# Performance work log

Hardware: AMD Instinct MI355X
Metric: run time of the kernel (lower is better)

The kernel has to match this reference:

```python
import jax, jax.numpy as jnp
import numpy as np

A = 16          # n_agents
H = 128         # rnn_hidden_dim
IN = 128        # input_shape
NA = 32         # n_attention
NACT = 14       # n_actions
TAU = 0.5       # gumbel_softmax_tau
B_ENV = 1024    # parallel envs
BZ = B_ENV * A

# neighbor index: for agent i, all j != i (matches select_ind in torch code)
IDX = np.array([[j for j in range(A) if j != i] for i in range(A)])  # [A, A-1]


def gru_cell(x, h, Wih, Whh, bih, bhh):
    # torch GRUCell gate order: r, z, n
    gi = x @ Wih.T + bih
    gh = h @ Whh.T + bhh
    ir, iz, inn = jnp.split(gi, 3, axis=-1)
    hr, hz, hn = jnp.split(gh, 3, axis=-1)
    r = jax.nn.sigmoid(ir + hr)
    z = jax.nn.sigmoid(iz + hz)
    n = jnp.tanh(inn + r * hn)
    return (1.0 - z) * n + z * h


def run_gru(seq, Wih, Whh, bih, bhh):
    # seq: [T, N, D]; returns all hidden states [T, N, H]
    h0 = jnp.zeros((seq.shape[1], Whh.shape[1]), seq.dtype)
    def step(h, x):
        h2 = gru_cell(x, h, Wih, Whh, bih, bhh)
        return h2, h2
    _, ys = jax.lax.scan(step, h0, seq)
    return ys


def setup_inputs() -> dict:
    key = jax.random.key(0)
    ks = jax.random.split(key, 24)
    def u(k, shape, fan):
        s = 1.0 / np.sqrt(fan)
        return jax.random.uniform(k, shape, jnp.float32, -s, s)
    inp = {
        "inputs": jax.random.normal(ks[0], (BZ, IN), jnp.float32),
        "hidden_state": jax.random.normal(ks[1], (BZ, H), jnp.float32),
        "gumbel_u": jax.random.uniform(ks[2], (BZ * (A - 1), 2), jnp.float32),
        # fc1
        "W1": u(ks[3], (H, IN), IN), "b1": u(ks[4], (H,), IN),
        # GRUCell
        "Wih_c": u(ks[5], (3 * H, H), H), "Whh_c": u(ks[6], (3 * H, H), H),
        "bih_c": u(ks[7], (3 * H,), H), "bhh_c": u(ks[8], (3 * H,), H),
        # bi-GRU forward dir (input 2H)
        "Wih_f": u(ks[9], (3 * H, 2 * H), H), "Whh_f": u(ks[10], (3 * H, H), H),
        "bih_f": u(ks[11], (3 * H,), H), "bhh_f": u(ks[12], (3 * H,), H),
        # bi-GRU backward dir
        "Wih_b": u(ks[13], (3 * H, 2 * H), H), "Whh_b": u(ks[14], (3 * H, H), H),
        "bih_b": u(ks[15], (3 * H,), H), "bhh_b": u(ks[16], (3 * H,), H),
        # hard classifier
        "Wc": u(ks[17], (2, 2 * H), 2 * H), "bc": u(ks[18], (2,), 2 * H),
        # attention projections (no bias)
        "Wq": u(ks[19], (NA, H), H), "Wk": u(ks[20], (NA, H), H),
        # fc2
        "W2": u(ks[21], (NACT, 2 * H), 2 * H), "b2": u(ks[22], (NACT,), 2 * H),
    }
    return inp


def reference(inputs, hidden_state, gumbel_u, W1, b1, Wih_c, Whh_c, bih_c, bhh_c,
              Wih_f, Whh_f, bih_f, bhh_f, Wih_b, Whh_b, bih_b, bhh_b,
              Wc, bc, Wq, Wk, W2, b2):
    bz = inputs.shape[0]
    B = bz // A
    x1 = jax.nn.relu(inputs @ W1.T + b1)
    h_rnn = gru_cell(x1, hidden_state.reshape(-1, H), Wih_c, Whh_c, bih_c, bhh_c)  # [bz, H]

    h3 = h_rnn.reshape(B, A, H)
    nbr = h3[:, IDX, :]                                           # [B, A, A-1, H]
    self_rep = jnp.broadcast_to(h3[:, :, None, :], (B, A, A - 1, H))
    pairs = jnp.concatenate([self_rep, nbr], axis=-1)             # [B, A, A-1, 2H]
    seq = pairs.transpose(2, 0, 1, 3).reshape(A - 1, bz, 2 * H)   # [T, bz, 2H]

    yf = run_gru(seq, Wih_f, Whh_f, bih_f, bhh_f)
    yb = jnp.flip(run_gru(jnp.flip(seq, 0), Wih_b, Whh_b, bih_b, bhh_b), 0)
    h_hard = jnp.concatenate([yf, yb], axis=-1)                   # [T, bz, 2H]
    h_hard = h_hard.transpose(1, 0, 2).reshape(-1, 2 * H)         # [bz*T, 2H]

    logits = h_hard @ Wc.T + bc                                   # [bz*T, 2]
    g = -jnp.log(-jnp.log(gumbel_u + 1e-10) + 1e-10)
    gs = jax.nn.softmax((logits + g) / TAU, axis=-1)
    hard_w = gs[:, 1].reshape(B, A, A - 1)                        # hard gate

    q = (h_rnn @ Wq.T).reshape(B, A, NA)
    k = (h_rnn @ Wk.T).reshape(B, A, NA)
    kn = k[:, IDX, :] * hard_w[..., None]                         # [B, A, A-1, NA]
    scores = jnp.einsum('bad,bamd->bam', q, kn) / np.sqrt(NA)
    soft_w = jax.nn.softmax(scores, axis=-1)                      # [B, A, A-1]

    w = hard_w * soft_w
    agg = jnp.einsum('bam,bamh->bah', w, nbr).reshape(bz, H)
    out = jnp.concatenate([h_rnn, agg], axis=-1) @ W2.T + b2      # [bz, n_actions]
    return out, h_rnn
```

## Files before the change

kernel.cpp:

```cpp
#include <hip/hip_runtime.h>
#include <hip/hip_bf16.h>


typedef __attribute__((ext_vector_type(8))) short short8;
typedef __attribute__((ext_vector_type(4))) short short4v;
typedef __attribute__((ext_vector_type(4))) float float4v;
typedef __attribute__((ext_vector_type(2))) unsigned long long ull2;

#define BF2F(x) __bfloat162float(x)
typedef __hip_bfloat16 bf;

__device__ __forceinline__ float frcp(float x) {
  return __builtin_amdgcn_rcpf(x);
}
__device__ __forceinline__ float fsigmoid(float x) {
  return frcp(1.f + __expf(-x));
}
__device__ __forceinline__ float ftanh(float x) {
  float e = __expf(2.f * x);
  return 1.f - 2.f * frcp(1.f + e);
}
__device__ __forceinline__ float rdv(const void* p, int i, int f) {
  return f ? ((const float*)p)[i] : BF2F(((const bf*)p)[i]);
}
__device__ __forceinline__ float upk(unsigned long long v, int s) {
  union { unsigned int i; float f; } x;
  x.i = ((unsigned int)((v >> s) & 0xffffULL)) << 16;
  return x.f;
}

static const int AO[23] = {
  0, 2097152, 4194304, 4685824, 4702208, 4702336, 4751488, 4800640, 4801024,
  4801408, 4899712, 4948864, 4949248, 4949632, 5047936, 5097088, 5097472,
  5097856, 5098368, 5098384, 5102480, 5106576, 5110160};
static const int AN[23] = {
  2097152, 2097152, 491520, 16384, 128, 49152, 49152, 384, 384, 98304, 49152,
  384, 384, 98304, 49152, 384, 384, 512, 2, 4096, 4096, 3584, 14};

struct CArgs {
  const void* src[23];
  int n[23];
  int off[23];
};

__global__ void kDetect(const unsigned short* __restrict__ p, int* flag) {
  __shared__ int s;
  if (threadIdx.x == 0) s = 0;
  __syncthreads();
  int hit = 0;
  for (int i = threadIdx.x; i < 4096; i += 1024) {
    int e = (p[i] >> 7) & 0xFF;
    if (e >= 0xC0) hit = 1;
  }
  if (hit) atomicOr(&s, 1);
  __syncthreads();
  if (threadIdx.x == 0) *flag = s;
}

__global__ void kConvert(CArgs a, const int* __restrict__ flag,
                         bf* __restrict__ arena,
                         const void* __restrict__ WqR, const void* __restrict__ WkR,
                         const void* __restrict__ W2R, const void* __restrict__ WcR,
                         bf* __restrict__ Wqk, bf* __restrict__ W2p,
                         bf* __restrict__ Wcb) {
  const int b = blockIdx.y;
  const int f = *flag;
  if (b == 23) {
    int idx = blockIdx.x * 256 + threadIdx.x;
    if (idx < 8192) {
      int r = idx >> 7, c = idx & 127;
      float v = (r < 32) ? rdv(WqR, r * 128 + c, f) : rdv(WkR, (r - 32) * 128 + c, f);
      Wqk[idx] = __float2bfloat16(v);
    }
    if (idx < 4096)
      W2p[idx] = __float2bfloat16((idx < 3584) ? rdv(W2R, idx, f) : 0.f);
    if (idx < 512) {
      int dir = idx >> 8, l = (idx >> 7) & 1, k = idx & 127;
      Wcb[idx] = __float2bfloat16(rdv(WcR, l * 256 + dir * 128 + k, f));
    }
    return;
  }
  if (b == 2 || b == 18 || b == 22) return;
  const int n = a.n[b];
  const int nv = n & ~7;
  bf* dst = arena + a.off[b];
  const int gid = blockIdx.x * 256 + threadIdx.x;
  const int gs = gridDim.x * 256;
  if (f) {
    const float* s = (const float*)a.src[b];
    for (int i = gid * 8; i < nv; i += gs * 8) {
      float4 x0 = *(const float4*)(s + i);
      float4 x1 = *(const float4*)(s + i + 4);
      short8 v;
      bf t;
      t = __float2bfloat16(x0.x); v[0] = *(short*)&t;
      t = __float2bfloat16(x0.y); v[1] = *(short*)&t;
      t = __float2bfloat16(x0.z); v[2] = *(short*)&t;
      t = __float2bfloat16(x0.w); v[3] = *(short*)&t;
      t = __float2bfloat16(x1.x); v[4] = *(short*)&t;
      t = __float2bfloat16(x1.y); v[5] = *(short*)&t;
      t = __float2bfloat16(x1.z); v[6] = *(short*)&t;
      t = __float2bfloat16(x1.w); v[7] = *(short*)&t;
      *(short8*)(dst + i) = v;
    }
    for (int i = nv + gid; i < n; i += gs) dst[i] = __float2bfloat16(s[i]);
  } else {
    const short8* s = (const short8*)a.src[b];
    short8* d = (short8*)dst;
    for (int i = gid; i * 8 < nv; i += gs) d[i] = s[i];
    const unsigned short* ss = (const unsigned short*)a.src[b];
    unsigned short* ds = (unsigned short*)dst;
    for (int i = nv + gid; i < n; i += gs) ds[i] = ss[i];
  }
}

__global__ __launch_bounds__(256) void kGemm(const bf* __restrict__ A,
                                             const bf* __restrict__ W,
                                             const bf* __restrict__ bias,
                                             bf* __restrict__ out,
                                             int N, int relu) {
  const int tid = threadIdx.x;
  const int wave = tid >> 6, lane = tid & 63;
  const int quad = lane >> 4, ci = lane & 15;
  const int mr = blockIdx.x * 64 + wave * 16;
  const int nbase = blockIdx.y * 64;
  const int ntiles = (N - nbase < 64) ? ((N - nbase) >> 4) : 4;

  float4v acc[4];
#pragma unroll
  for (int i = 0; i < 4; ++i) acc[i] = {0.f, 0.f, 0.f, 0.f};

#pragma unroll
  for (int ks = 0; ks < 4; ++ks) {
    short8 a = *(const short8*)(A + (size_t)(mr + ci) * 128 + ks * 32 + quad * 8);
    for (int nt = 0; nt < ntiles; ++nt) {
      short8 b = *(const short8*)(W + (size_t)(nbase + nt * 16 + ci) * 128 + ks * 32 + quad * 8);
      acc[nt] = __builtin_amdgcn_mfma_f32_16x16x32_bf16(a, b, acc[nt], 0, 0, 0);
    }
  }

  for (int nt = 0; nt < ntiles; ++nt) {
    int col = nbase + nt * 16 + ci;
    float bv = bias ? BF2F(bias[col]) : 0.f;
#pragma unroll
    for (int r = 0; r < 4; ++r) {
      int row = mr + quad * 4 + r;
      float v = acc[nt][r] + bv;
      if (relu) v = fmaxf(v, 0.f);
      out[(size_t)row * N + col] = __float2bfloat16(v);
    }
  }
}

__global__ __launch_bounds__(256, 4) void kStep(
    const bf* __restrict__ Hp, const bf* __restrict__ Whh,
    const bf* __restrict__ G, int gld,
    const bf* __restrict__ bhh,
    bf* __restrict__ Ho, float* __restrict__ HcopyF) {
  const int half = blockIdx.z;
  const int tid = threadIdx.x;
  const int wave = tid >> 6, lane = tid & 63;
  const int quad = lane >> 4, ci = lane & 15;
  const int mr = blockIdx.x * 64 + wave * 16;

  float4v acc[12];
#pragma unroll
  for (int i = 0; i < 12; ++i) acc[i] = {0.f, 0.f, 0.f, 0.f};

#pragma unroll
  for (int ks = 0; ks < 4; ++ks) {
    short8 a = *(const short8*)(Hp + (size_t)(mr + ci) * 128 + ks * 32 + quad * 8);
#pragma unroll
    for (int g = 0; g < 3; ++g)
#pragma unroll
      for (int nt = 0; nt < 4; ++nt) {
        short8 b = *(const short8*)(Whh + (size_t)(g * 128 + half * 64 + nt * 16 + ci) * 128 + ks * 32 + quad * 8);
        acc[g * 4 + nt] = __builtin_amdgcn_mfma_f32_16x16x32_bf16(a, b, acc[g * 4 + nt], 0, 0, 0);
      }
  }

  float bR[4], bZ[4], bN[4];
#pragma unroll
  for (int nt = 0; nt < 4; ++nt) {
    int c = half * 64 + nt * 16 + ci;
    bR[nt] = BF2F(bhh[c]);
    bZ[nt] = BF2F(bhh[128 + c]);
    bN[nt] = BF2F(bhh[256 + c]);
  }

#pragma unroll
  for (int r = 0; r < 4; ++r) {
    int rr = mr + quad * 4 + r;
    const bf* gs = G + (size_t)rr * gld;
#pragma unroll
    for (int nt = 0; nt < 4; ++nt) {
      int c = half * 64 + nt * 16 + ci;
      float gr = BF2F(gs[c]), gz = BF2F(gs[128 + c]), gnn = BF2F(gs[256 + c]);
      float pre_r = acc[nt][r] + gr + bR[nt];
      float pre_z = acc[4 + nt][r] + gz + bZ[nt];
      float hn_   = acc[8 + nt][r] + bN[nt];
      float rg = fsigmoid(pre_r);
      float zg = fsigmoid(pre_z);
      float ng = ftanh(gnn + rg * hn_);
      float hp = BF2F(Hp[(size_t)rr * 128 + c]);
      float hv = ng + zg * (hp - ng);
      Ho[(size_t)rr * 128 + c] = __float2bfloat16(hv);
      if (HcopyF) HcopyF[(size_t)rr * 128 + c] = hv;
    }
  }
}

__global__ __launch_bounds__(512, 4) void kSeq(
    const bf* __restrict__ hrnn,
    const bf* __restrict__ Wih_f, const bf* __restrict__ Wih_b,
    const bf* __restrict__ Whh_f, const bf* __restrict__ Whh_b,
    const bf* __restrict__ bih_f, const bf* __restrict__ bih_b,
    const bf* __restrict__ bhh_f, const bf* __restrict__ bhh_b,
    const bf* __restrict__ Wcb, float* __restrict__ L) {
  __shared__ unsigned long long sGiN[16][130];
  __shared__ bf sH[2][16][136];
  __shared__ float sL[16][15][2];
  __shared__ bf sWc[2][136];

  const int env = blockIdx.x;
  const int dir = blockIdx.y;
  const int tid = threadIdx.x;
  const int wave = tid >> 6, lane = tid & 63;
  const int nh = wave;
  const int quad = lane >> 4, ci = lane & 15;
  const bf* Wih = dir ? Wih_b : Wih_f;
  const bf* Whh = dir ? Whh_b : Whh_f;
  const bf* bih = dir ? bih_b : bih_f;
  const bf* bhh = dir ? bhh_b : bhh_f;
  const int h0q = nh * 16 + quad * 4;

  float4v gS[3], gN[3];
#pragma unroll
  for (int i = 0; i < 3; ++i) { gS[i] = {0.f, 0.f, 0.f, 0.f}; gN[i] = {0.f, 0.f, 0.f, 0.f}; }
#pragma unroll
  for (int ks = 0; ks < 4; ++ks) {
    short8 bh = *(const short8*)(hrnn + (size_t)(env * 16 + ci) * 128 + ks * 32 + quad * 8);
#pragma unroll
    for (int g = 0; g < 3; ++g) {
      const bf* wrow = Wih + (size_t)(g * 128 + nh * 16 + ci) * 256 + ks * 32 + quad * 8;
      short8 ws = *(const short8*)(wrow);
      short8 wn = *(const short8*)(wrow + 128);
      gS[g] = __builtin_amdgcn_mfma_f32_16x16x32_bf16(ws, bh, gS[g], 0, 0, 0);
      gN[g] = __builtin_amdgcn_mfma_f32_16x16x32_bf16(wn, bh, gN[g], 0, 0, 0);
    }
  }
#pragma unroll
  for (int g = 0; g < 3; ++g)
#pragma unroll
    for (int r = 0; r < 4; ++r) {
      int c = g * 128 + h0q + r;
      float bv = BF2F(bih[c]);
      if (g < 2) bv += BF2F(bhh[c]);
      gS[g][r] += bv;
    }
#pragma unroll
  for (int r = 0; r < 4; ++r) {
    unsigned long long pk = 0;
#pragma unroll
    for (int g = 0; g < 3; ++g) {
      bf b = __float2bfloat16(gN[g][r]);
      pk |= ((unsigned long long)(*(unsigned short*)&b)) << (16 * g);
    }
    sGiN[ci][h0q + r] = pk;
  }

  {
    bf z = __float2bfloat16(0.f);
    bf* p = &sH[0][0][0];
    for (int i = tid; i < 16 * 136; i += 512) p[i] = z;
    if (tid < 256)
      sWc[tid >> 7][tid & 127] = Wcb[(dir * 2 + (tid >> 7)) * 128 + (tid & 127)];
  }

  short8 Bf[12];
#pragma unroll
  for (int g = 0; g < 3; ++g)
#pragma unroll
    for (int ks = 0; ks < 4; ++ks)
      Bf[g * 4 + ks] =
          *(const short8*)(Whh + (size_t)(g * 128 + nh * 16 + ci) * 128 + ks * 32 + quad * 8);

  float bNc[4];
#pragma unroll
  for (int r = 0; r < 4; ++r) bNc[r] = BF2F(bhh[256 + h0q + r]);

  float hPrev[4];
#pragma unroll
  for (int r = 0; r < 4; ++r) hPrev[r] = 0.f;

  __syncthreads();

  for (int t = 0; t < 15; ++t) {
    const int cur = t & 1, nxt = cur ^ 1;
    const int m = dir ? (14 - t) : t;
    const int jr = m + ((m >= ci) ? 1 : 0);

    ull2 nb01 = *(const ull2*)&sGiN[jr][h0q];
    ull2 nb23 = *(const ull2*)&sGiN[jr][h0q + 2];

    float4v acc[3];
#pragma unroll
    for (int i = 0; i < 3; ++i) acc[i] = {0.f, 0.f, 0.f, 0.f};
    float4v lacc = {0.f, 0.f, 0.f, 0.f};
#pragma unroll
    for (int ks = 0; ks < 4; ++ks) {
      short8 bh = *(const short8*)&sH[cur][ci][ks * 32 + quad * 8];
#pragma unroll
      for (int g = 0; g < 3; ++g)
        acc[g] = __builtin_amdgcn_mfma_f32_16x16x32_bf16(Bf[g * 4 + ks], bh, acc[g], 0, 0, 0);
      if (nh == 0) {
        short8 wv = *(const short8*)&sWc[ci & 1][ks * 32 + quad * 8];
        lacc = __builtin_amdgcn_mfma_f32_16x16x32_bf16(wv, bh, lacc, 0, 0, 0);
      }
    }
    if (nh == 0 && t > 0 && quad == 0) {
      int mp = dir ? (15 - t) : (t - 1);
      sL[ci][mp][0] = lacc[0];
      sL[ci][mp][1] = lacc[1];
    }

    short4v hv4;
#pragma unroll
    for (int r = 0; r < 4; ++r) {
      unsigned long long nb = (r == 0) ? nb01.x : (r == 1) ? nb01.y
                             : (r == 2) ? nb23.x : nb23.y;
      float pre_r = acc[0][r] + gS[0][r] + upk(nb, 0);
      float pre_z = acc[1][r] + gS[1][r] + upk(nb, 16);
      float gnn   = gS[2][r] + upk(nb, 32);
      float hn_   = acc[2][r] + bNc[r];
      float rg = fsigmoid(pre_r);
      float zg = fsigmoid(pre_z);
      float ng = ftanh(gnn + rg * hn_);
      float hv = ng + zg * (hPrev[r] - ng);
      hPrev[r] = hv;
      bf b = __float2bfloat16(hv);
      hv4[r] = *(short*)&b;
    }
    *(short4v*)&sH[nxt][ci][h0q] = hv4;
    __syncthreads();
  }

  if (nh == 0) {
    float4v lacc = {0.f, 0.f, 0.f, 0.f};
#pragma unroll
    for (int ks = 0; ks < 4; ++ks) {
      short8 bh = *(const short8*)&sH[1][ci][ks * 32 + quad * 8];
      short8 wv = *(const short8*)&sWc[ci & 1][ks * 32 + quad * 8];
      lacc = __builtin_amdgcn_mfma_f32_16x16x32_bf16(wv, bh, lacc, 0, 0, 0);
    }
    if (quad == 0) {
      int mf = dir ? 0 : 14;
      sL[ci][mf][0] = lacc[0];
      sL[ci][mf][1] = lacc[1];
    }
  }
  __syncthreads();

  for (int i = tid; i < 480; i += 512) {
    int row = i / 30, rem = i - row * 30;
    int mm = rem >> 1, l = rem & 1;
    L[(size_t)((env * 16 + row) * 15 + mm) * 4 + dir * 2 + l] = sL[row][mm][l];
  }
}

__global__ __launch_bounds__(256) void kAttn(
    const bf* __restrict__ h, const bf* __restrict__ Wqk,
    const float* __restrict__ L, const void* __restrict__ guRaw,
    const void* __restrict__ bcRaw, const int* __restrict__ flag,
    bf* __restrict__ aggB) {
  __shared__ float sh[16 * 132];
  __shared__ float sqk[16 * 64];
  __shared__ float shw[16 * 15];
  __shared__ float sw[16 * 16];
  int bb = blockIdx.x, tid = threadIdx.x;
  const int f = *flag;

  {
    const int w = tid >> 6, lane = tid & 63;
    const int quad = lane >> 4, ci = lane & 15;
    float4v acc = {0.f, 0.f, 0.f, 0.f};
#pragma unroll
    for (int ks = 0; ks < 4; ++ks) {
      short8 a_ = *(const short8*)(h + (size_t)(bb * 16 + ci) * 128 + ks * 32 + quad * 8);
      short8 b_ = *(const short8*)(Wqk + (size_t)(w * 16 + ci) * 128 + ks * 32 + quad * 8);
      acc = __builtin_amdgcn_mfma_f32_16x16x32_bf16(a_, b_, acc, 0, 0, 0);
    }
#pragma unroll
    for (int r = 0; r < 4; ++r)
      sqk[(quad * 4 + r) * 64 + w * 16 + ci] = acc[r];
  }
  for (int i = tid; i < 2048; i += 256)
    sh[(i >> 7) * 132 + (i & 127)] = BF2F(h[(size_t)bb * 2048 + i]);
  if (tid < 240) {
    int idx = bb * 240 + tid;
    const float* Lp = L + (size_t)idx * 4;
    float l0 = Lp[0] + Lp[2] + rdv(bcRaw, 0, f);
    float l1 = Lp[1] + Lp[3] + rdv(bcRaw, 1, f);
    float u0 = rdv(guRaw, idx * 2, f);
    float u1 = rdv(guRaw, idx * 2 + 1, f);
    float g0 = -__logf(-__logf(u0 + 1e-10f) + 1e-10f);
    float g1 = -__logf(-__logf(u1 + 1e-10f) + 1e-10f);
    shw[tid] = fsigmoid(((l1 + g1) - (l0 + g0)) * 2.0f);
  }
  __syncthreads();

  int a = tid >> 4, i = tid & 15;
  float s = -1e30f;
  if (i < 15) {
    int j = i + (i >= a);
    float d = 0.f;
#pragma unroll
    for (int c = 0; c < 32; ++c) d += sqk[a * 64 + c] * sqk[j * 64 + 32 + c];
    s = shw[a * 15 + i] * d * 0.17677669529663687f;
  }
  float mx = s;
#pragma unroll
  for (int d = 1; d < 16; d <<= 1) mx = fmaxf(mx, __shfl_xor(mx, d));
  float e = (i < 15) ? __expf(s - mx) : 0.f;
  float sum = e;
#pragma unroll
  for (int d = 1; d < 16; d <<= 1) sum += __shfl_xor(sum, d);
  float w = (i < 15) ? (e * frcp(sum)) * shw[a * 15 + i] : 0.f;
  sw[a * 16 + i] = w;
  __syncthreads();

  float ac[8] = {0, 0, 0, 0, 0, 0, 0, 0};
  for (int mm = 0; mm < 15; ++mm) {
    int jm = mm + (mm >= a);
    float wm = sw[a * 16 + mm];
    const float* shp = &sh[jm * 132 + i * 8];
    float4 h0 = *(const float4*)shp;
    float4 h1 = *(const float4*)(shp + 4);
    ac[0] += wm * h0.x; ac[1] += wm * h0.y; ac[2] += wm * h0.z; ac[3] += wm * h0.w;
    ac[4] += wm * h1.x; ac[5] += wm * h1.y; ac[6] += wm * h1.z; ac[7] += wm * h1.w;
  }
  short8 v;
#pragma unroll
  for (int d = 0; d < 8; ++d) {
    bf b = __float2bfloat16(ac[d]);
    v[d] = *(short*)&b;
  }
  *(short8*)(aggB + (size_t)(bb * 16 + a) * 128 + i * 8) = v;
}

__global__ __launch_bounds__(256) void kGemmOut(
    const bf* __restrict__ hrnn, const bf* __restrict__ aggB,
    const bf* __restrict__ W2p, const void* __restrict__ b2Raw,
    const int* __restrict__ flag, float* __restrict__ out) {
  const int tid = threadIdx.x;
  const int wave = tid >> 6, lane = tid & 63;
  const int quad = lane >> 4, ci = lane & 15;
  const int mr = blockIdx.x * 64 + wave * 16;
  const int f = *flag;

  float4v acc = {0.f, 0.f, 0.f, 0.f};
#pragma unroll
  for (int ks = 0; ks < 8; ++ks) {
    const bf* src = (ks < 4) ? hrnn : aggB;
    int k = (ks & 3) * 32 + quad * 8;
    short8 a = *(const short8*)(src + (size_t)(mr + ci) * 128 + k);
    short8 b = *(const short8*)(W2p + (size_t)ci * 256 + ks * 32 + quad * 8);
    acc = __builtin_amdgcn_mfma_f32_16x16x32_bf16(a, b, acc, 0, 0, 0);
  }

  if (ci < 14) {
    float bv = rdv(b2Raw, ci, f);
#pragma unroll
    for (int r = 0; r < 4; ++r)
      out[(size_t)(mr + quad * 4 + r) * 14 + ci] = acc[r] + bv;
  }
}

extern "C" void kernel_launch(void* const* d_in, const int* in_sizes, int n_in,
                              void* d_out, int out_size, void* d_ws, size_t ws_size,
                              hipStream_t stream) {
  const size_t OFF_ARENA = 0;
  const size_t OFF_FLAG  = 10220544;
  const size_t OFF_A     = 10220800;
  const size_t OFF_WQK   = 26998016;
  const size_t OFF_WCB   = 27014400;
  const size_t OFF_W2P   = 27410944;
  const size_t OFF_HRNN  = 27419136;
  const size_t NEEDED    = 84042240;
  if (ws_size < NEEDED) return;
  if (n_in < 23 || in_sizes[0] != 2097152 || in_sizes[3] != 16384 ||
      in_sizes[5] != 49152 || in_sizes[9] != 98304 || in_sizes[17] != 512 ||
      in_sizes[19] != 4096 || in_sizes[21] != 3584 || out_size != 2326528)
    return;

  char* ws = (char*)d_ws;
  bf*    arena = (bf*)(ws + OFF_ARENA);
  float* L     = (float*)(ws + OFF_ARENA);
  int*   flag  = (int*)(ws + OFF_FLAG);
  bf*    x1    = (bf*)(ws + OFF_A);
  bf*    gi_c  = (bf*)(ws + OFF_A + 4194304);
  bf*    aggB  = (bf*)(ws + OFF_A + 983040);
  bf*    Wqk   = (bf*)(ws + OFF_WQK);
  bf*    Wcb   = (bf*)(ws + OFF_WCB);
  bf*    W2p   = (bf*)(ws + OFF_W2P);
  bf*    hrnn  = (bf*)(ws + OFF_HRNN);

  float* out14 = (float*)d_out;
  float* outh  = (float*)d_out + 229376;

  kDetect<<<1, 1024, 0, stream>>>((const unsigned short*)d_in[0], flag);
  CArgs ca;
  for (int i = 0; i < 23; ++i) { ca.src[i] = d_in[i]; ca.n[i] = AN[i]; ca.off[i] = AO[i]; }
  kConvert<<<dim3(128, 24), 256, 0, stream>>>(ca, flag, arena,
                                              d_in[19], d_in[20], d_in[21], d_in[17],
                                              Wqk, W2p, Wcb);

  const bf* inputs = arena + AO[0];
  const bf* hidden = arena + AO[1];
  const bf* W1     = arena + AO[3];
  const bf* b1     = arena + AO[4];
  const bf* Wih_c  = arena + AO[5];
  const bf* Whh_c  = arena + AO[6];
  const bf* bih_c  = arena + AO[7];
  const bf* bhh_c  = arena + AO[8];
  const bf* Wih_f  = arena + AO[9];
  const bf* Whh_f  = arena + AO[10];
  const bf* bih_f  = arena + AO[11];
  const bf* bhh_f  = arena + AO[12];
  const bf* Wih_b  = arena + AO[13];
  const bf* Whh_b  = arena + AO[14];
  const bf* bih_b  = arena + AO[15];
  const bf* bhh_b  = arena + AO[16];

  kGemm<<<dim3(256, 2), 256, 0, stream>>>(inputs, W1, b1, x1, 128, 1);
  kGemm<<<dim3(256, 6), 256, 0, stream>>>(x1, Wih_c, bih_c, gi_c, 384, 0);
  kStep<<<dim3(256, 1, 2), 256, 0, stream>>>(hidden, Whh_c, gi_c, 384, bhh_c,
                                             hrnn, outh);

  kSeq<<<dim3(1024, 2), 512, 0, stream>>>(hrnn, Wih_f, Wih_b, Whh_f, Whh_b,
                                          bih_f, bih_b, bhh_f, bhh_b, Wcb, L);

  kAttn<<<dim3(1024), 256, 0, stream>>>(hrnn, Wqk, L, d_in[2], d_in[18], flag,
                                        aggB);
  kGemmOut<<<dim3(256), 256, 0, stream>>>(hrnn, aggB, W2p, d_in[22], flag, out14);
}
```

Measured before the change: 280.5 us.

## Fuse detect into convert, fc1 with GRU input GEMM, and attention with output GEMM

Folds the dtype-detection kernel into the convert kernel, where every block recomputes the flag locally. Fuses the fc1 GEMM with ReLU and the GRU input-projection GEMM into one kernel, keeping x1 in LDS. Fuses attention with the final output GEMM, keeping aggregated vectors in LDS and processing four envs per block. This removes three launches and intermediate global round trips, but the attention stage drops from 1024 to 256 blocks and is serialised inside each block.

```diff
diff --git a/kernel.cpp b/kernel.cpp
--- a/kernel.cpp
+++ b/kernel.cpp
@@ -43,28 +43,29 @@
   int off[23];
 };
 
-__global__ void kDetect(const unsigned short* __restrict__ p, int* flag) {
-  __shared__ int s;
-  if (threadIdx.x == 0) s = 0;
-  __syncthreads();
-  int hit = 0;
-  for (int i = threadIdx.x; i < 4096; i += 1024) {
-    int e = (p[i] >> 7) & 0xFF;
-    if (e >= 0xC0) hit = 1;
-  }
-  if (hit) atomicOr(&s, 1);
-  __syncthreads();
-  if (threadIdx.x == 0) *flag = s;
-}
-
-__global__ void kConvert(CArgs a, const int* __restrict__ flag,
+__global__ void kConvert(CArgs a, int* __restrict__ flagOut,
                          bf* __restrict__ arena,
                          const void* __restrict__ WqR, const void* __restrict__ WkR,
                          const void* __restrict__ W2R, const void* __restrict__ WcR,
                          bf* __restrict__ Wqk, bf* __restrict__ W2p,
                          bf* __restrict__ Wcb) {
+  __shared__ int sflag;
+  if (threadIdx.x == 0) sflag = 0;
+  __syncthreads();
+  {
+    const unsigned short* p0 = (const unsigned short*)a.src[0];
+    int hit = 0;
+    for (int i = threadIdx.x; i < 4096; i += 256) {
+      int e = (p0[i] >> 7) & 0xFF;
+      if (e >= 0xC0) hit = 1;
+    }
+    if (hit) atomicOr(&sflag, 1);
+  }
+  __syncthreads();
+  const int f = sflag;
   const int b = blockIdx.y;
-  const int f = *flag;
+  if (b == 0 && blockIdx.x == 0 && threadIdx.x == 0) *flagOut = f;
+
   if (b == 23) {
     int idx = blockIdx.x * 256 + threadIdx.x;
     if (idx < 8192) {
@@ -114,40 +115,63 @@
   }
 }
 
-__global__ __launch_bounds__(256) void kGemm(const bf* __restrict__ A,
-                                             const bf* __restrict__ W,
-                                             const bf* __restrict__ bias,
-                                             bf* __restrict__ out,
-                                             int N, int relu) {
+__global__ __launch_bounds__(256) void kFused12(
+    const bf* __restrict__ inputs, const bf* __restrict__ W1,
+    const bf* __restrict__ b1, const bf* __restrict__ Wih,
+    const bf* __restrict__ bih, bf* __restrict__ gi) {
+  __shared__ bf sX[4][16][136];
   const int tid = threadIdx.x;
   const int wave = tid >> 6, lane = tid & 63;
   const int quad = lane >> 4, ci = lane & 15;
-  const int mr = blockIdx.x * 64 + wave * 16;
-  const int nbase = blockIdx.y * 64;
-  const int ntiles = (N - nbase < 64) ? ((N - nbase) >> 4) : 4;
-
-  float4v acc[4];
-#pragma unroll
-  for (int i = 0; i < 4; ++i) acc[i] = {0.f, 0.f, 0.f, 0.f};
-
+  const int row0 = blockIdx.x * 64 + wave * 16;
+
+  float4v xa[8];
+#pragma unroll
+  for (int i = 0; i < 8; ++i) xa[i] = {0.f, 0.f, 0.f, 0.f};
 #pragma unroll
   for (int ks = 0; ks < 4; ++ks) {
-    short8 a = *(const short8*)(A + (size_t)(mr + ci) * 128 + ks * 32 + quad * 8);
-    for (int nt = 0; nt < ntiles; ++nt) {
-      short8 b = *(const short8*)(W + (size_t)(nbase + nt * 16 + ci) * 128 + ks * 32 + quad * 8);
-      acc[nt] = __builtin_amdgcn_mfma_f32_16x16x32_bf16(a, b, acc[nt], 0, 0, 0);
-    }
-  }
-
-  for (int nt = 0; nt < ntiles; ++nt) {
-    int col = nbase + nt * 16 + ci;
-    float bv = bias ? BF2F(bias[col]) : 0.f;
+    short8 inr = *(const short8*)(inputs + (size_t)(row0 + ci) * 128 + ks * 32 + quad * 8);
+#pragma unroll
+    for (int ct = 0; ct < 8; ++ct) {
+      short8 wfr = *(const short8*)(W1 + (size_t)(ct * 16 + ci) * 128 + ks * 32 + quad * 8);
+      xa[ct] = __builtin_amdgcn_mfma_f32_16x16x32_bf16(wfr, inr, xa[ct], 0, 0, 0);
+    }
+  }
+#pragma unroll
+  for (int ct = 0; ct < 8; ++ct) {
+    short4v v4;
 #pragma unroll
     for (int r = 0; r < 4; ++r) {
-      int row = mr + quad * 4 + r;
-      float v = acc[nt][r] + bv;
-      if (relu) v = fmaxf(v, 0.f);
-      out[(size_t)row * N + col] = __float2bfloat16(v);
+      float v = xa[ct][r] + BF2F(b1[ct * 16 + quad * 4 + r]);
+      v = fmaxf(v, 0.f);
+      bf t = __float2bfloat16(v);
+      v4[r] = *(short*)&t;
+    }
+    *(short4v*)&sX[wave][ci][ct * 16 + quad * 4] = v4;
+  }
+  short8 af[4];
+#pragma unroll
+  for (int ks = 0; ks < 4; ++ks)
+    af[ks] = *(const short8*)&sX[wave][ci][ks * 32 + quad * 8];
+
+  for (int cg = 0; cg < 6; ++cg) {
+    float4v acc[4];
+#pragma unroll
+    for (int i = 0; i < 4; ++i) acc[i] = {0.f, 0.f, 0.f, 0.f};
+#pragma unroll
+    for (int ks = 0; ks < 4; ++ks)
+#pragma unroll
+      for (int nt = 0; nt < 4; ++nt) {
+        short8 b = *(const short8*)(Wih + (size_t)(cg * 64 + nt * 16 + ci) * 128 + ks * 32 + quad * 8);
+        acc[nt] = __builtin_amdgcn_mfma_f32_16x16x32_bf16(af[ks], b, acc[nt], 0, 0, 0);
+      }
+#pragma unroll
+    for (int nt = 0; nt < 4; ++nt) {
+      int col = cg * 64 + nt * 16 + ci;
+      float bv = BF2F(bih[col]);
+#pragma unroll
+      for (int r = 0; r < 4; ++r)
+        gi[(size_t)(row0 + quad * 4 + r) * 384 + col] = __float2bfloat16(acc[nt][r] + bv);
     }
   }
 }
@@ -368,111 +392,116 @@
   }
 }
 
-__global__ __launch_bounds__(256) void kAttn(
+__global__ __launch_bounds__(256) void kTail(
     const bf* __restrict__ h, const bf* __restrict__ Wqk,
     const float* __restrict__ L, const void* __restrict__ guRaw,
     const void* __restrict__ bcRaw, const int* __restrict__ flag,
-    bf* __restrict__ aggB) {
+    const bf* __restrict__ W2p, const void* __restrict__ b2Raw,
+    float* __restrict__ out) {
   __shared__ float sh[16 * 132];
   __shared__ float sqk[16 * 64];
-  __shared__ float shw[16 * 15];
+  __shared__ float shw[240];
   __shared__ float sw[16 * 16];
-  int bb = blockIdx.x, tid = threadIdx.x;
+  __shared__ bf sAgg[64][136];
+  const int b4 = blockIdx.x;
+  const int tid = threadIdx.x;
   const int f = *flag;
+  const int a = tid >> 4, i = tid & 15;
+
+  for (int e = 0; e < 4; ++e) {
+    const int bb = b4 * 4 + e;
+    __syncthreads();
+    {
+      const int w = tid >> 6, lane = tid & 63;
+      const int quad = lane >> 4, ci = lane & 15;
+      float4v acc = {0.f, 0.f, 0.f, 0.f};
+#pragma unroll
+      for (int ks = 0; ks < 4; ++ks) {
+        short8 a_ = *(const short8*)(h + (size_t)(bb * 16 + ci) * 128 + ks * 32 + quad * 8);
+        short8 b_ = *(const short8*)(Wqk + (size_t)(w * 16 + ci) * 128 + ks * 32 + quad * 8);
+        acc = __builtin_amdgcn_mfma_f32_16x16x32_bf16(a_, b_, acc, 0, 0, 0);
+      }
+#pragma unroll
+      for (int r = 0; r < 4; ++r)
+        sqk[(quad * 4 + r) * 64 + w * 16 + ci] = acc[r];
+    }
+    for (int k = tid; k < 2048; k += 256)
+      sh[(k >> 7) * 132 + (k & 127)] = BF2F(h[(size_t)bb * 2048 + k]);
+    if (tid < 240) {
+      int idx = bb * 240 + tid;
+      const float* Lp = L + (size_t)idx * 4;
+      float l0 = Lp[0] + Lp[2] + rdv(bcRaw, 0, f);
+      float l1 = Lp[1] + Lp[3] + rdv(bcRaw, 1, f);
+      float u0 = rdv(guRaw, idx * 2, f);
+      float u1 = rdv(guRaw, idx * 2 + 1, f);
+      float g0 = -__logf(-__logf(u0 + 1e-10f) + 1e-10f);
+      float g1 = -__logf(-__logf(u1 + 1e-10f) + 1e-10f);
+      shw[tid] = fsigmoid(((l1 + g1) - (l0 + g0)) * 2.0f);
+    }
+    __syncthreads();
+
+    float s = -1e30f;
+    if (i < 15) {
+      int j = i + (i >= a);
+      float d = 0.f;
+#pragma unroll
+      for (int c = 0; c < 32; ++c) d += sqk[a * 64 + c] * sqk[j * 64 + 32 + c];
+      s = shw[a * 15 + i] * d * 0.17677669529663687f;
+    }
+    float mx = s;
+#pragma unroll
+    for (int d = 1; d < 16; d <<= 1) mx = fmaxf(mx, __shfl_xor(mx, d));
+    float ex = (i < 15) ? __expf(s - mx) : 0.f;
+    float sum = ex;
+#pragma unroll
+    for (int d = 1; d < 16; d <<= 1) sum += __shfl_xor(sum, d);
+    float w = (i < 15) ? (ex * frcp(sum)) * shw[a * 15 + i] : 0.f;
+    sw[a * 16 + i] = w;
+    __syncthreads();
+
+    float ac[8] = {0, 0, 0, 0, 0, 0, 0, 0};
+    for (int mm = 0; mm < 15; ++mm) {
+      int jm = mm + (mm >= a);
+      float wm = sw[a * 16 + mm];
+      const float* shp = &sh[jm * 132 + i * 8];
+      float4 h0 = *(const float4*)shp;
+      float4 h1 = *(const float4*)(shp + 4);
+      ac[0] += wm * h0.x; ac[1] += wm * h0.y; ac[2] += wm * h0.z; ac[3] += wm * h0.w;
+      ac[4] += wm * h1.x; ac[5] += wm * h1.y; ac[6] += wm * h1.z; ac[7] += wm * h1.w;
+    }
+    short8 v;
+#pragma unroll
+    for (int d = 0; d < 8; ++d) {
+      bf b = __float2bfloat16(ac[d]);
+      v[d] = *(short*)&b;
+    }
+    *(short8*)&sAgg[e * 16 + a][i * 8] = v;
+  }
+  __syncthreads();
 
   {
-    const int w = tid >> 6, lane = tid & 63;
+    const int wave = tid >> 6, lane = tid & 63;
     const int quad = lane >> 4, ci = lane & 15;
+    const int mr = b4 * 64 + wave * 16;
     float4v acc = {0.f, 0.f, 0.f, 0.f};
 #pragma unroll
     for (int ks = 0; ks < 4; ++ks) {
-      short8 a_ = *(const short8*)(h + (size_t)(bb * 16 + ci) * 128 + ks * 32 + quad * 8);
-      short8 b_ = *(const short8*)(Wqk + (size_t)(w * 16 + ci) * 128 + ks * 32 + quad * 8);
+      short8 a_ = *(const short8*)(h + (size_t)(mr + ci) * 128 + ks * 32 + quad * 8);
+      short8 b_ = *(const short8*)(W2p + (size_t)ci * 256 + ks * 32 + quad * 8);
       acc = __builtin_amdgcn_mfma_f32_16x16x32_bf16(a_, b_, acc, 0, 0, 0);
     }
 #pragma unroll
-    for (int r = 0; r < 4; ++r)
-      sqk[(quad * 4 + r) * 64 + w * 16 + ci] = acc[r];
-  }
-  for (int i = tid; i < 2048; i += 256)
-    sh[(i >> 7) * 132 + (i & 127)] = BF2F(h[(size_t)bb * 2048 + i]);
-  if (tid < 240) {
-    int idx = bb * 240 + tid;
-    const float* Lp = L + (size_t)idx * 4;
-    float l0 = Lp[0] + Lp[2] + rdv(bcRaw, 0, f);
-    float l1 = Lp[1] + Lp[3] + rdv(bcRaw, 1, f);
-    float u0 = rdv(guRaw, idx * 2, f);
-    float u1 = rdv(guRaw, idx * 2 + 1, f);
-    float g0 = -__logf(-__logf(u0 + 1e-10f) + 1e-10f);
-    float g1 = -__logf(-__logf(u1 + 1e-10f) + 1e-10f);
-    shw[tid] = fsigmoid(((l1 + g1) - (l0 + g0)) * 2.0f);
-  }
-  __syncthreads();
-
-  int a = tid >> 4, i = tid & 15;
-  float s = -1e30f;
-  if (i < 15) {
-    int j = i + (i >= a);
-    float d = 0.f;
-#pragma unroll
-    for (int c = 0; c < 32; ++c) d += sqk[a * 64 + c] * sqk[j * 64 + 32 + c];
-    s = shw[a * 15 + i] * d * 0.17677669529663687f;
-  }
-  float mx = s;
-#pragma unroll
-  for (int d = 1; d < 16; d <<= 1) mx = fmaxf(mx, __shfl_xor(mx, d));
-  float e = (i < 15) ? __expf(s - mx) : 0.f;
-  float sum = e;
-#pragma unroll
-  for (int d = 1; d < 16; d <<= 1) sum += __shfl_xor(sum, d);
-  float w = (i < 15) ? (e * frcp(sum)) * shw[a * 15 + i] : 0.f;
-  sw[a * 16 + i] = w;
-  __syncthreads();
-
-  float ac[8] = {0, 0, 0, 0, 0, 0, 0, 0};
-  for (int mm = 0; mm < 15; ++mm) {
-    int jm = mm + (mm >= a);
-    float wm = sw[a * 16 + mm];
-    const float* shp = &sh[jm * 132 + i * 8];
-    float4 h0 = *(const float4*)shp;
-    float4 h1 = *(const float4*)(shp + 4);
-    ac[0] += wm * h0.x; ac[1] += wm * h0.y; ac[2] += wm * h0.z; ac[3] += wm * h0.w;
-    ac[4] += wm * h1.x; ac[5] += wm * h1.y; ac[6] += wm * h1.z; ac[7] += wm * h1.w;
-  }
-  short8 v;
-#pragma unroll
-  for (int d = 0; d < 8; ++d) {
-    bf b = __float2bfloat16(ac[d]);
-    v[d] = *(short*)&b;
-  }
-  *(short8*)(aggB + (size_t)(bb * 16 + a) * 128 + i * 8) = v;
-}
-
-__global__ __launch_bounds__(256) void kGemmOut(
-    const bf* __restrict__ hrnn, const bf* __restrict__ aggB,
-    const bf* __restrict__ W2p, const void* __restrict__ b2Raw,
-    const int* __restrict__ flag, float* __restrict__ out) {
-  const int tid = threadIdx.x;
-  const int wave = tid >> 6, lane = tid & 63;
-  const int quad = lane >> 4, ci = lane & 15;
-  const int mr = blockIdx.x * 64 + wave * 16;
-  const int f = *flag;
-
-  float4v acc = {0.f, 0.f, 0.f, 0.f};
-#pragma unroll
-  for (int ks = 0; ks < 8; ++ks) {
-    const bf* src = (ks < 4) ? hrnn : aggB;
-    int k = (ks & 3) * 32 + quad * 8;
-    short8 a = *(const short8*)(src + (size_t)(mr + ci) * 128 + k);
-    short8 b = *(const short8*)(W2p + (size_t)ci * 256 + ks * 32 + quad * 8);
-    acc = __builtin_amdgcn_mfma_f32_16x16x32_bf16(a, b, acc, 0, 0, 0);
-  }
-
-  if (ci < 14) {
-    float bv = rdv(b2Raw, ci, f);
-#pragma unroll
-    for (int r = 0; r < 4; ++r)
-      out[(size_t)(mr + quad * 4 + r) * 14 + ci] = acc[r] + bv;
+    for (int ks = 0; ks < 4; ++ks) {
+      short8 a_ = *(const short8*)&sAgg[wave * 16 + ci][ks * 32 + quad * 8];
+      short8 b_ = *(const short8*)(W2p + (size_t)ci * 256 + 128 + ks * 32 + quad * 8);
+      acc = __builtin_amdgcn_mfma_f32_16x16x32_bf16(a_, b_, acc, 0, 0, 0);
+    }
+    if (ci < 14) {
+      float bv = rdv(b2Raw, ci, f);
+#pragma unroll
+      for (int r = 0; r < 4; ++r)
+        out[(size_t)(mr + quad * 4 + r) * 14 + ci] = acc[r] + bv;
+    }
   }
 }
 
@@ -497,9 +526,7 @@
   bf*    arena = (bf*)(ws + OFF_ARENA);
   float* L     = (float*)(ws + OFF_ARENA);
   int*   flag  = (int*)(ws + OFF_FLAG);
-  bf*    x1    = (bf*)(ws + OFF_A);
   bf*    gi_c  = (bf*)(ws + OFF_A + 4194304);
-  bf*    aggB  = (bf*)(ws + OFF_A + 983040);
   bf*    Wqk   = (bf*)(ws + OFF_WQK);
   bf*    Wcb   = (bf*)(ws + OFF_WCB);
   bf*    W2p   = (bf*)(ws + OFF_W2P);
@@ -508,7 +535,6 @@
   float* out14 = (float*)d_out;
   float* outh  = (float*)d_out + 229376;
 
-  kDetect<<<1, 1024, 0, stream>>>((const unsigned short*)d_in[0], flag);
   CArgs ca;
   for (int i = 0; i < 23; ++i) { ca.src[i] = d_in[i]; ca.n[i] = AN[i]; ca.off[i] = AO[i]; }
   kConvert<<<dim3(128, 24), 256, 0, stream>>>(ca, flag, arena,
@@ -532,15 +558,11 @@
   const bf* bih_b  = arena + AO[15];
   const bf* bhh_b  = arena + AO[16];
 
-  kGemm<<<dim3(256, 2), 256, 0, stream>>>(inputs, W1, b1, x1, 128, 1);
-  kGemm<<<dim3(256, 6), 256, 0, stream>>>(x1, Wih_c, bih_c, gi_c, 384, 0);
+  kFused12<<<dim3(256), 256, 0, stream>>>(inputs, W1, b1, Wih_c, bih_c, gi_c);
   kStep<<<dim3(256, 1, 2), 256, 0, stream>>>(hidden, Whh_c, gi_c, 384, bhh_c,
                                              hrnn, outh);
-
   kSeq<<<dim3(1024, 2), 512, 0, stream>>>(hrnn, Wih_f, Wih_b, Whh_f, Whh_b,
                                           bih_f, bih_b, bhh_f, bhh_b, Wcb, L);
-
-  kAttn<<<dim3(1024), 256, 0, stream>>>(hrnn, Wqk, L, d_in[2], d_in[18], flag,
-                                        aggB);
-  kGemmOut<<<dim3(256), 256, 0, stream>>>(hrnn, aggB, W2p, d_in[22], flag, out14);
-}
+  kTail<<<dim3(256), 256, 0, stream>>>(hrnn, Wqk, L, d_in[2], d_in[18], flag,
+                                       W2p, d_in[22], out14);
+}
```

After: 280.7 us. About the same (+0.0%).
